# Kernel optimization log

Hardware: AMD Instinct MI355X
Metric: run time of the kernel (lower is better)

Reference implementation:

```python
import jax, jax.numpy as jnp
import numpy as np

H = 1024      # hidden_size
NH = 16       # num_heads
DK = H // NH  # head dim


def setup_inputs() -> dict:
    key = jax.random.key(0)
    ks = jax.random.split(key, 5)
    s = 0.02
    return {
        "x": jax.random.normal(ks[0], (4, 2048, H), dtype=jnp.float32),
        "W_attn": jax.random.normal(ks[1], (H, 3 * H), dtype=jnp.float32) * s,
        "b_attn": jnp.zeros((3 * H,), dtype=jnp.float32),
        "W_proj": jax.random.normal(ks[2], (H, H), dtype=jnp.float32) * s,
        "b_proj": jnp.zeros((H,), dtype=jnp.float32),
    }


def reference(x, W_attn, b_attn, W_proj, b_proj):
    B, S, _ = x.shape
    qkv = x @ W_attn + b_attn                      # [B,S,3H]
    q, k, v = jnp.split(qkv, 3, axis=-1)
    # split heads -> [B,NH,S,DK]
    def heads(t):
        return t.reshape(B, S, NH, DK).transpose(0, 2, 1, 3)
    q, k, v = heads(q), heads(k), heads(v)
    scores = jnp.einsum("bhqd,bhkd->bhqk", q, k) / jnp.sqrt(jnp.float32(DK))
    causal = jnp.triu(jnp.full((S, S), -jnp.inf, dtype=scores.dtype), k=1)
    scores = scores + causal                        # additive causal mask
    attn = jax.nn.softmax(scores, axis=-1)
    out = jnp.einsum("bhqk,bhkd->bhqd", attn, v)   # [B,NH,S,DK]
    out = out.transpose(0, 2, 1, 3).reshape(B, S, H)
    return out @ W_proj + b_proj
```

## Files before the change

kernel.cpp:

```cpp
#include <hip/hip_runtime.h>
#include <hip/hip_bf16.h>


typedef __attribute__((ext_vector_type(8))) short bhalf8;
typedef __attribute__((ext_vector_type(4))) float floatx4;
typedef __attribute__((ext_vector_type(16))) float floatx16;

#define SB 2048
#define HB 1024
#define H3 3072

#if __has_builtin(__builtin_amdgcn_exp2f)
#define EXP2(x) __builtin_amdgcn_exp2f(x)
#else
#define EXP2(x) exp2f(x)
#endif

__device__ __forceinline__ float bf2f(unsigned short u) {
  union { unsigned int i; float f; } c; c.i = ((unsigned int)u) << 16; return c.f;
}
__device__ __forceinline__ unsigned short f2bf(float f) {
  union { float f; unsigned int i; } c; c.f = f;
  unsigned int r = c.i + 0x7fffu + ((c.i >> 16) & 1u);
  return (unsigned short)(r >> 16);
}
__device__ __forceinline__ int pkbf(float lo, float hi_) {
  union { __hip_bfloat162 h; int i; } u;
  u.h = __float22bfloat162_rn(make_float2(lo, hi_));
  return u.i;
}

__device__ __forceinline__ void gl_lds16(const unsigned short* g, unsigned short* l) {
  __builtin_amdgcn_global_load_lds(
      (const __attribute__((address_space(1))) unsigned int*)g,
      (__attribute__((address_space(3))) unsigned int*)l, 16, 0, 0);
}

#define REP16(OP) OP(0) OP(1) OP(2) OP(3) OP(4) OP(5) OP(6) OP(7) \
                  OP(8) OP(9) OP(10) OP(11) OP(12) OP(13) OP(14) OP(15)

__global__ void cvt_f32_bf16(const float* __restrict__ in, unsigned short* __restrict__ out, int n) {
  int i = (blockIdx.x * blockDim.x + threadIdx.x) * 4;
  if (i >= n) return;
  float4 v = *(const float4*)(in + i);
  ushort4 o;
  o.x = f2bf(v.x); o.y = f2bf(v.y); o.z = f2bf(v.z); o.w = f2bf(v.w);
  *(ushort4*)(out + i) = o;
}

__global__ void transpose_cvt(const float* __restrict__ in, unsigned short* __restrict__ out,
                              int K, int N) {
  __shared__ float tile[32][33];
  int n0 = blockIdx.x * 32, k0 = blockIdx.y * 32;
  for (int i = threadIdx.y; i < 32; i += 8)
    tile[i][threadIdx.x] = in[(size_t)(k0 + i) * N + n0 + threadIdx.x];
  __syncthreads();
  for (int i = threadIdx.y; i < 32; i += 8)
    out[(size_t)(n0 + i) * K + k0 + threadIdx.x] = f2bf(tile[threadIdx.x][i]);
}

__global__ void transpose_v(const unsigned short* __restrict__ qkv,
                            unsigned short* __restrict__ Vt) {
  __shared__ unsigned short tile[32][33];
  const int bh = blockIdx.z;
  const int b = bh >> 4, h = bh & 15;
  const int s0 = blockIdx.x * 32;
  const int d0 = blockIdx.y * 32;
  const int tx = threadIdx.x;
  const unsigned short* src = qkv + (size_t)(b * SB + s0) * H3 + 2 * HB + h * 64 + d0;
  for (int i = threadIdx.y; i < 32; i += 8)
    tile[i][tx] = src[(size_t)i * H3 + tx];
  __syncthreads();
  unsigned short* dst = Vt + ((size_t)bh * 64 + d0) * SB + s0;
  for (int i = threadIdx.y; i < 32; i += 8)
    dst[(size_t)i * SB + tx] = tile[tx][i];
}

template <bool FUSEV>
__global__ __launch_bounds__(512, 2) void gemm_v9(
    const unsigned short* __restrict__ A,
    const unsigned short* __restrict__ Bt,
    const float* __restrict__ bias,
    unsigned short* __restrict__ C,
    unsigned short* __restrict__ Vt,
    int M, int N, int K) {
  __shared__ __align__(16) unsigned short Sm[3 * 20480];
  const int tid = threadIdx.x;
  const int lane = tid & 63;
  const int w = tid >> 6;
  const int l15 = lane & 15, l4 = lane >> 4;
  const int wm = w >> 2, wn = w & 3;

  const int gx = gridDim.x;
  int lin = blockIdx.y * gx + blockIdx.x;
  const int cpx = (gx * gridDim.y) >> 3;
  lin = (lin & 7) * cpx + (lin >> 3);
  const int m0 = (lin / gx) * 256;
  const int n0 = (lin % gx) * 384;

  const int rb0 = tid >> 2;
  const int co = (((tid & 3) ^ ((tid >> 3) & 3)) * 8);
  const unsigned short* pA0 = A + (size_t)(m0 + rb0) * K + co;
  const unsigned short* pA1 = pA0 + (size_t)128 * K;
  const unsigned short* pB0 = Bt + (size_t)(n0 + rb0) * K + co;
  const unsigned short* pB1 = pB0 + (size_t)128 * K;
  const unsigned short* pB2 = pB0 + (size_t)256 * K;

  const int ra0 = wm * 128 + l15;
  const int ab0 = ra0 * 64 + ((l4 ^ ((ra0 >> 1) & 3)) << 4);
  const int rbq = wn * 96 + l15;
  const int bb0 = 16384 + rbq * 64 + ((l4 ^ ((rbq >> 1) & 3)) << 4);

  const floatx4 zero = {0.f, 0.f, 0.f, 0.f};
  floatx4 acc[8][6];
#pragma unroll
  for (int i = 0; i < 8; ++i)
#pragma unroll
    for (int j = 0; j < 6; ++j) acc[i][j] = zero;

#define STAGE_A(k0, ss)                                                 \
  { gl_lds16(pA0 + (k0), Sm + (ss) + tid * 8);                          \
    gl_lds16(pA1 + (k0), Sm + (ss) + (tid + 512) * 8); }
#define STAGE_B(k0, ss)                                                 \
  { gl_lds16(pB0 + (k0), Sm + (ss) + 8192 + tid * 8);                   \
    gl_lds16(pB1 + (k0), Sm + (ss) + 8192 + (tid + 512) * 8);           \
    gl_lds16(pB2 + (k0), Sm + (ss) + 8192 + (tid + 1024) * 8); }

  const int NT = K >> 5;
  STAGE_A(0, 0)      STAGE_B(0, 0)
  STAGE_A(32, 20480) STAGE_B(32, 20480)
  int sb = 0;
  int ss = 40960;

  for (int t = 0; t < NT; ++t) {
    if (t < NT - 1) asm volatile("s_waitcnt vmcnt(5)" ::: "memory");
    else            asm volatile("s_waitcnt vmcnt(0)" ::: "memory");
    __builtin_amdgcn_s_barrier();

    const char* LB = (const char*)(Sm + sb);
    const int k2 = (t + 2) * 32;
    const bool st = (t + 2 < NT);

    bhalf8 a0 = *(const bhalf8*)(LB + ab0);
    bhalf8 a1 = *(const bhalf8*)(LB + ab0 + 1024);
    bhalf8 a2 = *(const bhalf8*)(LB + ab0 + 2048);
    bhalf8 a3 = *(const bhalf8*)(LB + ab0 + 3072);
    bhalf8 b0 = *(const bhalf8*)(LB + bb0);
    bhalf8 b1 = *(const bhalf8*)(LB + bb0 + 1024);
    bhalf8 b2 = *(const bhalf8*)(LB + bb0 + 2048);
    bhalf8 b3 = *(const bhalf8*)(LB + bb0 + 3072);
    bhalf8 b4 = *(const bhalf8*)(LB + bb0 + 4096);
    bhalf8 b5 = *(const bhalf8*)(LB + bb0 + 5120);
    if (st) STAGE_A(k2, ss)
    __builtin_amdgcn_s_setprio(1);
#define MROW(i, av)                                                              \
    acc[i][0] = __builtin_amdgcn_mfma_f32_16x16x32_bf16(av, b0, acc[i][0], 0, 0, 0); \
    acc[i][1] = __builtin_amdgcn_mfma_f32_16x16x32_bf16(av, b1, acc[i][1], 0, 0, 0); \
    acc[i][2] = __builtin_amdgcn_mfma_f32_16x16x32_bf16(av, b2, acc[i][2], 0, 0, 0); \
    acc[i][3] = __builtin_amdgcn_mfma_f32_16x16x32_bf16(av, b3, acc[i][3], 0, 0, 0); \
    acc[i][4] = __builtin_amdgcn_mfma_f32_16x16x32_bf16(av, b4, acc[i][4], 0, 0, 0); \
    acc[i][5] = __builtin_amdgcn_mfma_f32_16x16x32_bf16(av, b5, acc[i][5], 0, 0, 0);
    MROW(0, a0) MROW(1, a1) MROW(2, a2) MROW(3, a3)
    __builtin_amdgcn_s_setprio(0);
    __builtin_amdgcn_s_barrier();

    bhalf8 a4 = *(const bhalf8*)(LB + ab0 + 4096);
    bhalf8 a5 = *(const bhalf8*)(LB + ab0 + 5120);
    bhalf8 a6 = *(const bhalf8*)(LB + ab0 + 6144);
    bhalf8 a7 = *(const bhalf8*)(LB + ab0 + 7168);
    if (st) STAGE_B(k2, ss)
    __builtin_amdgcn_s_setprio(1);
    MROW(4, a4) MROW(5, a5) MROW(6, a6) MROW(7, a7)
#undef MROW
    __builtin_amdgcn_s_setprio(0);

    sb = (sb == 40960) ? 0 : sb + 20480;
    ss = (ss == 40960) ? 0 : ss + 20480;
  }
#undef STAGE_A
#undef STAGE_B

#pragma unroll
  for (int i = 0; i < 8; ++i) {
    int row = m0 + wm * 128 + i * 16 + (l4 << 2);
#pragma unroll
    for (int j = 0; j < 6; ++j) {
      int col = n0 + wn * 96 + j * 16 + l15;
      float bb = bias[col];
      if (!FUSEV || col < 2048) {
#pragma unroll
        for (int r = 0; r < 4; ++r)
          C[(size_t)(row + r) * N + col] = f2bf(acc[i][j][r] + bb);
      } else {
        int vc = col - 2048;
        int h = vc >> 6, dk = vc & 63;
        int b = row >> 11, s = row & 2047;
        ushort4 pv;
        pv.x = f2bf(acc[i][j][0] + bb);
        pv.y = f2bf(acc[i][j][1] + bb);
        pv.z = f2bf(acc[i][j][2] + bb);
        pv.w = f2bf(acc[i][j][3] + bb);
        *(ushort4*)(Vt + ((size_t)((b * 16 + h) * 64 + dk)) * SB + s) = pv;
      }
    }
  }
}

template <bool F32OUT>
__global__ __launch_bounds__(512, 4) void gemm_v6(
    const unsigned short* __restrict__ A,
    const unsigned short* __restrict__ Bt,
    const float* __restrict__ bias,
    void* __restrict__ Cv,
    int M, int N, int K) {
  __shared__ __align__(16) unsigned short Sm[3 * 12288];
  const int tid = threadIdx.x;
  const int lane = tid & 63;
  const int w = tid >> 6;
  const int l15 = lane & 15, l4 = lane >> 4;
  const int wr = (w >> 1) * 64;
  const int wc = (w & 1) * 64;

  const int gx = gridDim.x;
  int lin = blockIdx.y * gx + blockIdx.x;
  const int cpx = (gx * gridDim.y) >> 3;
  lin = (lin & 7) * cpx + (lin >> 3);
  const int m0 = (lin / gx) * 256;
  const int n0 = (lin % gx) * 128;

  const int idx0 = tid, idx1 = tid + 512;
  const unsigned short* pA0 = A + (size_t)(m0 + (idx0 >> 2)) * K + (((idx0 & 3) ^ ((idx0 >> 3) & 3)) * 8);
  const unsigned short* pA1 = A + (size_t)(m0 + (idx1 >> 2)) * K + (((idx1 & 3) ^ ((idx1 >> 3) & 3)) * 8);
  const unsigned short* pB  = Bt + (size_t)(n0 + (tid >> 2)) * K + (((tid & 3) ^ ((tid >> 3) & 3)) * 8);

  int abyte[4], bbyte[4];
#pragma unroll
  for (int i = 0; i < 4; ++i) {
    int ra = wr + i * 16 + l15;
    abyte[i] = ra * 64 + ((l4 ^ ((ra >> 1) & 3)) << 4);
    int rb = wc + i * 16 + l15;
    bbyte[i] = 16384 + rb * 64 + ((l4 ^ ((rb >> 1) & 3)) << 4);
  }

  const floatx4 zero = {0.f, 0.f, 0.f, 0.f};
  floatx4 acc[4][4];
#pragma unroll
  for (int i = 0; i < 4; ++i)
#pragma unroll
    for (int j = 0; j < 4; ++j) acc[i][j] = zero;

#define STAGE_A6(k0, sbase)                                             \
  { gl_lds16(pA0 + (k0), Sm + (sbase) + idx0 * 8);                      \
    gl_lds16(pA1 + (k0), Sm + (sbase) + idx1 * 8); }
#define STAGE_B6(k0, sbase)                                             \
  { gl_lds16(pB + (k0), Sm + (sbase) + 8192 + tid * 8); }

  const int NT = K >> 5;
  STAGE_A6(0, 0)  STAGE_B6(0, 0)
  STAGE_A6(32, 12288) STAGE_B6(32, 12288)
  int sb = 0;
  int ss = 24576;

  for (int t = 0; t < NT; ++t) {
    if (t < NT - 1) asm volatile("s_waitcnt vmcnt(3)" ::: "memory");
    else            asm volatile("s_waitcnt vmcnt(0)" ::: "memory");
    __builtin_amdgcn_s_barrier();

    const char* LB = (const char*)(Sm + sb);
    const int k2 = (t + 2) * 32;
    const bool st = (t + 2 < NT);

    bhalf8 a0 = *(const bhalf8*)(LB + abyte[0]);
    bhalf8 a1 = *(const bhalf8*)(LB + abyte[1]);
    bhalf8 b0 = *(const bhalf8*)(LB + bbyte[0]);
    bhalf8 b1 = *(const bhalf8*)(LB + bbyte[1]);
    bhalf8 b2 = *(const bhalf8*)(LB + bbyte[2]);
    bhalf8 b3 = *(const bhalf8*)(LB + bbyte[3]);
    if (st) STAGE_A6(k2, ss)
    __builtin_amdgcn_s_setprio(1);
    acc[0][0] = __builtin_amdgcn_mfma_f32_16x16x32_bf16(a0, b0, acc[0][0], 0, 0, 0);
    acc[0][1] = __builtin_amdgcn_mfma_f32_16x16x32_bf16(a0, b1, acc[0][1], 0, 0, 0);
    acc[0][2] = __builtin_amdgcn_mfma_f32_16x16x32_bf16(a0, b2, acc[0][2], 0, 0, 0);
    acc[0][3] = __builtin_amdgcn_mfma_f32_16x16x32_bf16(a0, b3, acc[0][3], 0, 0, 0);
    acc[1][0] = __builtin_amdgcn_mfma_f32_16x16x32_bf16(a1, b0, acc[1][0], 0, 0, 0);
    acc[1][1] = __builtin_amdgcn_mfma_f32_16x16x32_bf16(a1, b1, acc[1][1], 0, 0, 0);
    acc[1][2] = __builtin_amdgcn_mfma_f32_16x16x32_bf16(a1, b2, acc[1][2], 0, 0, 0);
    acc[1][3] = __builtin_amdgcn_mfma_f32_16x16x32_bf16(a1, b3, acc[1][3], 0, 0, 0);
    __builtin_amdgcn_s_setprio(0);
    __builtin_amdgcn_s_barrier();

    bhalf8 a2 = *(const bhalf8*)(LB + abyte[2]);
    bhalf8 a3 = *(const bhalf8*)(LB + abyte[3]);
    if (st) STAGE_B6(k2, ss)
    __builtin_amdgcn_s_setprio(1);
    acc[2][0] = __builtin_amdgcn_mfma_f32_16x16x32_bf16(a2, b0, acc[2][0], 0, 0, 0);
    acc[2][1] = __builtin_amdgcn_mfma_f32_16x16x32_bf16(a2, b1, acc[2][1], 0, 0, 0);
    acc[2][2] = __builtin_amdgcn_mfma_f32_16x16x32_bf16(a2, b2, acc[2][2], 0, 0, 0);
    acc[2][3] = __builtin_amdgcn_mfma_f32_16x16x32_bf16(a2, b3, acc[2][3], 0, 0, 0);
    acc[3][0] = __builtin_amdgcn_mfma_f32_16x16x32_bf16(a3, b0, acc[3][0], 0, 0, 0);
    acc[3][1] = __builtin_amdgcn_mfma_f32_16x16x32_bf16(a3, b1, acc[3][1], 0, 0, 0);
    acc[3][2] = __builtin_amdgcn_mfma_f32_16x16x32_bf16(a3, b2, acc[3][2], 0, 0, 0);
    acc[3][3] = __builtin_amdgcn_mfma_f32_16x16x32_bf16(a3, b3, acc[3][3], 0, 0, 0);
    __builtin_amdgcn_s_setprio(0);

    sb = (sb == 24576) ? 0 : sb + 12288;
    ss = (ss == 24576) ? 0 : ss + 12288;
  }
#undef STAGE_A6
#undef STAGE_B6

  float* Cf = (float*)Cv;
  unsigned short* Cb = (unsigned short*)Cv;
#pragma unroll
  for (int i = 0; i < 4; ++i) {
    int row = m0 + wr + i * 16 + (l4 << 2);
#pragma unroll
    for (int j = 0; j < 4; ++j) {
      int col = n0 + wc + j * 16 + l15;
      float bb = bias[col];
#pragma unroll
      for (int r = 0; r < 4; ++r) {
        float v = acc[i][j][r] + bb;
        size_t idx = (size_t)(row + r) * N + col;
        if constexpr (F32OUT) Cf[idx] = v;
        else Cb[idx] = f2bf(v);
      }
    }
  }
}

__global__ __launch_bounds__(256, 4) void flash_attn4(
    const unsigned short* __restrict__ qkv,
    const unsigned short* __restrict__ Vt,
    unsigned short* __restrict__ outp) {
  __shared__ __align__(16) unsigned short Sm[4 * 4096];

  const int tid = threadIdx.x;
  const int lane = tid & 63;
  const int w = tid >> 6;
  const int hi = lane >> 5;
  const int qc = lane & 31;
  const int bh = blockIdx.x;
  const int b = bh >> 4, h = bh & 15;
  const int qt = 15 - (int)blockIdx.y;
  const int wq0 = qt * 128 + w * 32;
  const size_t rowbase = (size_t)b * SB;
  const int qg = wq0 + qc;
  const int nt = 2 * qt + 2;

  bhalf8 qf[4];
  {
    const unsigned short* qp = qkv + (rowbase + qg) * H3 + h * 64 + hi * 8;
#pragma unroll
    for (int kk = 0; kk < 4; ++kk) {
      bhalf8 v = *(const bhalf8*)(qp + kk * 16);
      bhalf8 o;
#pragma unroll
      for (int j = 0; j < 8; ++j)
        o[j] = (short)f2bf(bf2f((unsigned short)v[j]) * 0.18033688f);
      qf[kk] = o;
    }
  }

  const floatx16 Z16 = {0,0,0,0,0,0,0,0,0,0,0,0,0,0,0,0};
  floatx16 acc0 = Z16, acc1 = Z16;
  float l_half = 0.f;

  const char* LB = (const char*)Sm;
  int koff[8];
#pragma unroll
  for (int kk = 0; kk < 4; ++kk) {
    int xo = (((2 * kk + hi) ^ (qc & 7)) << 4);
    koff[2 * kk]     = qc * 128 + xo;
    koff[2 * kk + 1] = (32 + qc) * 128 + xo;
  }

  const int srow = tid >> 3, schk = tid & 7;
  const int sxe = (schk ^ (srow & 7)) * 8;
  const unsigned short* kp = qkv + (rowbase + srow) * H3 + HB + h * 64 + sxe;
  const unsigned short* vp = Vt + ((size_t)bh * 64 + srow) * SB + sxe;

  {
    unsigned short* kb = Sm + tid * 8;
    gl_lds16(kp, kb);
    gl_lds16(kp + 32 * H3, kb + 2048);
    gl_lds16(vp, kb + 8192);
    gl_lds16(vp + 32 * SB, kb + 8192 + 2048);
  }

#define QKK(BUFB, kk)                                                              \
      { bhalf8 ka = *(const bhalf8*)(LB + (BUFB) + koff[2*(kk)]);                  \
        s0 = __builtin_amdgcn_mfma_f32_32x32x16_bf16(ka, qf[kk], s0, 0, 0, 0);     \
        bhalf8 kb2 = *(const bhalf8*)(LB + (BUFB) + koff[2*(kk)+1]);               \
        s1 = __builtin_amdgcn_mfma_f32_32x32x16_bf16(kb2, qf[kk], s1, 0, 0, 0); }
#define PVC(BUFB, c, pfv)                                                          \
      { bhalf8 va = *(const bhalf8*)(LB + 16384 + (BUFB) + koff[2*(c)]);           \
        acc0 = __builtin_amdgcn_mfma_f32_32x32x16_bf16(va, pfv, acc0, 0, 0, 0);    \
        bhalf8 vb2 = *(const bhalf8*)(LB + 16384 + (BUFB) + koff[2*(c)+1]);        \
        acc1 = __builtin_amdgcn_mfma_f32_32x32x16_bf16(vb2, pfv, acc1, 0, 0, 0); }
#define MSK0(r) { if (k0 + (((r)&3) + 8*((r)>>2)) + 4*hi > qg)      s0[r] = -3.0e38f; }
#define MSK1(r) { if (k0 + 32 + (((r)&3) + 8*((r)>>2)) + 4*hi > qg) s1[r] = -3.0e38f; }
#define PEXP(r) { s0[r] = EXP2(s0[r]); s1[r] = EXP2(s1[r]); rsx[(r)&3] += s0[r] + s1[r]; }
  union PW { int i[4]; bhalf8 v; };
#define PACK2(dst, sv, rb)                                               \
      { int A0 = pkbf(sv[rb + 0], sv[rb + 1]);                           \
        int A1 = pkbf(sv[rb + 2], sv[rb + 3]);                           \
        int B0 = pkbf(sv[rb + 4], sv[rb + 5]);                           \
        int B1 = pkbf(sv[rb + 6], sv[rb + 7]);                           \
        auto r0 = __builtin_amdgcn_permlane32_swap(A0, B0, false, false);\
        auto r1 = __builtin_amdgcn_permlane32_swap(A1, B1, false, false);\
        PW u;                                                            \
        u.i[0] = r0[0]; u.i[1] = r1[0];                                  \
        u.i[2] = r0[1]; u.i[3] = r1[1];                                  \
        dst = u.v; }

#define FLASH_COMPUTE(BUFB)                                                        \
    { floatx16 s0 = Z16, s1 = Z16;                                                 \
      __builtin_amdgcn_s_setprio(1);                                               \
      QKK(BUFB, 0) QKK(BUFB, 1) QKK(BUFB, 2) QKK(BUFB, 3)                          \
      __builtin_amdgcn_s_setprio(0);                                               \
      if (k0 + 63 > wq0) { REP16(MSK0) REP16(MSK1) }                               \
      float rsx[4] = {0.f, 0.f, 0.f, 0.f};                                         \
      REP16(PEXP)                                                                  \
      l_half += (rsx[0] + rsx[1]) + (rsx[2] + rsx[3]);                             \
      bhalf8 pf0, pf1, pf2, pf3;                                                   \
      PACK2(pf0, s0, 0) PACK2(pf1, s0, 8) PACK2(pf2, s1, 0) PACK2(pf3, s1, 8)      \
      __builtin_amdgcn_s_setprio(1);                                               \
      PVC(BUFB, 0, pf0) PVC(BUFB, 1, pf1) PVC(BUFB, 2, pf2) PVC(BUFB, 3, pf3)      \
      __builtin_amdgcn_s_setprio(0); }

#define DO_STEP(T, BUF)                                                            \
  { __syncthreads();                                                               \
    if ((T) + 1 < nt) {                                                            \
      kp += 64 * H3; vp += 64;                                                     \
      unsigned short* kb = Sm + (1 - (BUF)) * 4096 + tid * 8;                      \
      gl_lds16(kp, kb); gl_lds16(kp + 32 * H3, kb + 2048);                         \
      gl_lds16(vp, kb + 8192); gl_lds16(vp + 32 * SB, kb + 8192 + 2048);           \
    }                                                                              \
    const int k0 = (T) * 64;                                                       \
    if (k0 <= wq0 + 31) FLASH_COMPUTE((BUF) * 8192)                                \
  }

  for (int t = 0; t < nt; t += 2) {
    DO_STEP(t, 0)
    DO_STEP(t + 1, 1)
  }

  const float l_full = l_half + __shfl_xor(l_half, 32);
  const float inv_l = 1.f / l_full;
  unsigned short* op = outp + (rowbase + qg) * HB + h * 64;
#pragma unroll
  for (int tq = 0; tq < 4; ++tq) {
    ushort4 st;
    st.x = f2bf(acc0[4 * tq + 0] * inv_l);
    st.y = f2bf(acc0[4 * tq + 1] * inv_l);
    st.z = f2bf(acc0[4 * tq + 2] * inv_l);
    st.w = f2bf(acc0[4 * tq + 3] * inv_l);
    *(ushort4*)(op + 8 * tq + 4 * hi) = st;
    ushort4 su;
    su.x = f2bf(acc1[4 * tq + 0] * inv_l);
    su.y = f2bf(acc1[4 * tq + 1] * inv_l);
    su.z = f2bf(acc1[4 * tq + 2] * inv_l);
    su.w = f2bf(acc1[4 * tq + 3] * inv_l);
    *(ushort4*)(op + 32 + 8 * tq + 4 * hi) = su;
  }
}

extern "C" void kernel_launch(void* const* d_in, const int* in_sizes, int n_in,
                              void* d_out, int out_size, void* d_ws, size_t ws_size,
                              hipStream_t stream) {
  const float* x      = (const float*)d_in[0];
  const float* W_attn = (const float*)d_in[1];
  const float* b_attn = (const float*)d_in[2];
  const float* W_proj = (const float*)d_in[3];
  const float* b_proj = (const float*)d_in[4];
  float* out = (float*)d_out;

  char* ws = (char*)d_ws;
  unsigned short* x_bf    = (unsigned short*)(ws);
  unsigned short* Wt_attn = (unsigned short*)(ws + 16777216);
  unsigned short* Wt_proj = (unsigned short*)(ws + 23068672);
  unsigned short* qkv     = (unsigned short*)(ws + 25165824);
  unsigned short* attn    = (unsigned short*)(ws + 75497472);
  const bool fuse = ws_size >= (size_t)92274688 + 16777216;
  unsigned short* VtF = (unsigned short*)(ws + 92274688);
  unsigned short* Vt  = fuse ? VtF : x_bf;

  cvt_f32_bf16<<<8192, 256, 0, stream>>>(x, x_bf, 8192 * 1024);
  transpose_cvt<<<dim3(96, 32), dim3(32, 8), 0, stream>>>(W_attn, Wt_attn, 1024, 3072);
  transpose_cvt<<<dim3(32, 32), dim3(32, 8), 0, stream>>>(W_proj, Wt_proj, 1024, 1024);

  if (fuse) {
    gemm_v9<true><<<dim3(8, 32), 512, 0, stream>>>(x_bf, Wt_attn, b_attn, qkv, VtF,
                                                   8192, 3072, 1024);
  } else {
    gemm_v9<false><<<dim3(8, 32), 512, 0, stream>>>(x_bf, Wt_attn, b_attn, qkv, nullptr,
                                                    8192, 3072, 1024);
    transpose_v<<<dim3(64, 2, 64), dim3(32, 8), 0, stream>>>(qkv, Vt);
  }
  flash_attn4<<<dim3(64, 16), 256, 0, stream>>>(qkv, Vt, attn);
  gemm_v6<true><<<dim3(8, 32), 512, 0, stream>>>(attn, Wt_proj, b_proj, out,
                                                 8192, 1024, 1024);
}
```

Measured before the change: 145.9 us.

## Triple-buffer K/V tiles in flash attention with explicit vmcnt waits

Replaces the double-buffered K/V LDS staging in the attention kernel with a three-stage ring. Loads run two tiles ahead, and partial s_waitcnt vmcnt waits replace the full __syncthreads drain. The goal is to hide global-to-LDS load latency behind the MFMA compute. In exchange it uses 48KB of LDS per block and lowers the launch-bound occupancy hint from 4 to 3 blocks.

```diff
diff --git a/kernel.cpp b/kernel.cpp
--- a/kernel.cpp
+++ b/kernel.cpp
@@ -193,14 +193,14 @@
           C[(size_t)(row + r) * N + col] = f2bf(acc[i][j][r] + bb);
       } else {
         int vc = col - 2048;
-        int h = vc >> 6, dk = vc & 63;
-        int b = row >> 11, s = row & 2047;
+        int h2 = vc >> 6, dk = vc & 63;
+        int b2 = row >> 11, s = row & 2047;
         ushort4 pv;
         pv.x = f2bf(acc[i][j][0] + bb);
         pv.y = f2bf(acc[i][j][1] + bb);
         pv.z = f2bf(acc[i][j][2] + bb);
         pv.w = f2bf(acc[i][j][3] + bb);
-        *(ushort4*)(Vt + ((size_t)((b * 16 + h) * 64 + dk)) * SB + s) = pv;
+        *(ushort4*)(Vt + ((size_t)((b2 * 16 + h2) * 64 + dk)) * SB + s) = pv;
       }
     }
   }
@@ -329,11 +329,11 @@
   }
 }
 
-__global__ __launch_bounds__(256, 4) void flash_attn4(
+__global__ __launch_bounds__(256, 3) void flash_attn5(
     const unsigned short* __restrict__ qkv,
     const unsigned short* __restrict__ Vt,
     unsigned short* __restrict__ outp) {
-  __shared__ __align__(16) unsigned short Sm[4 * 4096];
+  __shared__ __align__(16) unsigned short Sm[3 * 8192];
 
   const int tid = threadIdx.x;
   const int lane = tid & 63;
@@ -366,7 +366,6 @@
   floatx16 acc0 = Z16, acc1 = Z16;
   float l_half = 0.f;
 
-  const char* LB = (const char*)Sm;
   int koff[8];
 #pragma unroll
   for (int kk = 0; kk < 4; ++kk) {
@@ -380,28 +379,53 @@
   const unsigned short* kp = qkv + (rowbase + srow) * H3 + HB + h * 64 + sxe;
   const unsigned short* vp = Vt + ((size_t)bh * 64 + srow) * SB + sxe;
 
-  {
-    unsigned short* kb = Sm + tid * 8;
-    gl_lds16(kp, kb);
-    gl_lds16(kp + 32 * H3, kb + 2048);
-    gl_lds16(vp, kb + 8192);
-    gl_lds16(vp + 32 * SB, kb + 8192 + 2048);
-  }
-
-#define QKK(BUFB, kk)                                                              \
-      { bhalf8 ka = *(const bhalf8*)(LB + (BUFB) + koff[2*(kk)]);                  \
-        s0 = __builtin_amdgcn_mfma_f32_32x32x16_bf16(ka, qf[kk], s0, 0, 0, 0);     \
-        bhalf8 kb2 = *(const bhalf8*)(LB + (BUFB) + koff[2*(kk)+1]);               \
-        s1 = __builtin_amdgcn_mfma_f32_32x32x16_bf16(kb2, qf[kk], s1, 0, 0, 0); }
-#define PVC(BUFB, c, pfv)                                                          \
-      { bhalf8 va = *(const bhalf8*)(LB + 16384 + (BUFB) + koff[2*(c)]);           \
-        acc0 = __builtin_amdgcn_mfma_f32_32x32x16_bf16(va, pfv, acc0, 0, 0, 0);    \
-        bhalf8 vb2 = *(const bhalf8*)(LB + 16384 + (BUFB) + koff[2*(c)+1]);        \
-        acc1 = __builtin_amdgcn_mfma_f32_32x32x16_bf16(vb2, pfv, acc1, 0, 0, 0); }
+#define STG(CS, KO)                                                              \
+  { unsigned short* kb = Sm + (CS) + tid * 8;                                    \
+    gl_lds16(kp + (size_t)(KO) * H3,        kb);                                 \
+    gl_lds16(kp + (size_t)((KO) + 32) * H3, kb + 2048);                          \
+    gl_lds16(vp + (KO),            kb + 4096);                                   \
+    gl_lds16(vp + (KO) + 32 * SB,  kb + 6144); }
+
+  STG(0, 0)
+  STG(8192, 64)
+  int cmp = 0;
+  int stg = 16384;
+
+  for (int t = 0; t < nt; ++t) {
+    if (t < nt - 1) asm volatile("s_waitcnt vmcnt(4)" ::: "memory");
+    else            asm volatile("s_waitcnt vmcnt(0)" ::: "memory");
+    __builtin_amdgcn_s_barrier();
+
+    if (t + 2 < nt) STG(stg, (t + 2) * 64)
+
+    const int k0 = t * 64;
+    if (k0 <= wq0 + 31) {
+      const char* Lc = (const char*)Sm + cmp * 2;
+
+      floatx16 s0 = Z16, s1 = Z16;
+      __builtin_amdgcn_s_setprio(1);
+#pragma unroll
+      for (int kk = 0; kk < 4; ++kk) {
+        bhalf8 ka  = *(const bhalf8*)(Lc + koff[2 * kk]);
+        s0 = __builtin_amdgcn_mfma_f32_32x32x16_bf16(ka, qf[kk], s0, 0, 0, 0);
+        bhalf8 kb2 = *(const bhalf8*)(Lc + koff[2 * kk + 1]);
+        s1 = __builtin_amdgcn_mfma_f32_32x32x16_bf16(kb2, qf[kk], s1, 0, 0, 0);
+      }
+      __builtin_amdgcn_s_setprio(0);
+
+      if (k0 + 63 > wq0) {
 #define MSK0(r) { if (k0 + (((r)&3) + 8*((r)>>2)) + 4*hi > qg)      s0[r] = -3.0e38f; }
 #define MSK1(r) { if (k0 + 32 + (((r)&3) + 8*((r)>>2)) + 4*hi > qg) s1[r] = -3.0e38f; }
+        REP16(MSK0)
+        REP16(MSK1)
+      }
+
+      float rsx[4] = {0.f, 0.f, 0.f, 0.f};
 #define PEXP(r) { s0[r] = EXP2(s0[r]); s1[r] = EXP2(s1[r]); rsx[(r)&3] += s0[r] + s1[r]; }
-  union PW { int i[4]; bhalf8 v; };
+      REP16(PEXP)
+      l_half += (rsx[0] + rsx[1]) + (rsx[2] + rsx[3]);
+
+      union PW { int i[4]; bhalf8 v; };
 #define PACK2(dst, sv, rb)                                               \
       { int A0 = pkbf(sv[rb + 0], sv[rb + 1]);                           \
         int A1 = pkbf(sv[rb + 2], sv[rb + 3]);                           \
@@ -413,38 +437,30 @@
         u.i[0] = r0[0]; u.i[1] = r1[0];                                  \
         u.i[2] = r0[1]; u.i[3] = r1[1];                                  \
         dst = u.v; }
-
-#define FLASH_COMPUTE(BUFB)                                                        \
-    { floatx16 s0 = Z16, s1 = Z16;                                                 \
-      __builtin_amdgcn_s_setprio(1);                                               \
-      QKK(BUFB, 0) QKK(BUFB, 1) QKK(BUFB, 2) QKK(BUFB, 3)                          \
-      __builtin_amdgcn_s_setprio(0);                                               \
-      if (k0 + 63 > wq0) { REP16(MSK0) REP16(MSK1) }                               \
-      float rsx[4] = {0.f, 0.f, 0.f, 0.f};                                         \
-      REP16(PEXP)                                                                  \
-      l_half += (rsx[0] + rsx[1]) + (rsx[2] + rsx[3]);                             \
-      bhalf8 pf0, pf1, pf2, pf3;                                                   \
-      PACK2(pf0, s0, 0) PACK2(pf1, s0, 8) PACK2(pf2, s1, 0) PACK2(pf3, s1, 8)      \
-      __builtin_amdgcn_s_setprio(1);                                               \
-      PVC(BUFB, 0, pf0) PVC(BUFB, 1, pf1) PVC(BUFB, 2, pf2) PVC(BUFB, 3, pf3)      \
-      __builtin_amdgcn_s_setprio(0); }
-
-#define DO_STEP(T, BUF)                                                            \
-  { __syncthreads();                                                               \
-    if ((T) + 1 < nt) {                                                            \
-      kp += 64 * H3; vp += 64;                                                     \
-      unsigned short* kb = Sm + (1 - (BUF)) * 4096 + tid * 8;                      \
-      gl_lds16(kp, kb); gl_lds16(kp + 32 * H3, kb + 2048);                         \
-      gl_lds16(vp, kb + 8192); gl_lds16(vp + 32 * SB, kb + 8192 + 2048);           \
-    }                                                                              \
-    const int k0 = (T) * 64;                                                       \
-    if (k0 <= wq0 + 31) FLASH_COMPUTE((BUF) * 8192)                                \
-  }
-
-  for (int t = 0; t < nt; t += 2) {
-    DO_STEP(t, 0)
-    DO_STEP(t + 1, 1)
-  }
+      bhalf8 pf0, pf1, pf2, pf3;
+      PACK2(pf0, s0, 0)
+      PACK2(pf1, s0, 8)
+      PACK2(pf2, s1, 0)
+      PACK2(pf3, s1, 8)
+
+      __builtin_amdgcn_s_setprio(1);
+#define PVC(c, pfv)                                                                  \
+      { bhalf8 va  = *(const bhalf8*)(Lc + 8192 + koff[2 * (c)]);                    \
+        acc0 = __builtin_amdgcn_mfma_f32_32x32x16_bf16(va, pfv, acc0, 0, 0, 0);      \
+        bhalf8 vb2 = *(const bhalf8*)(Lc + 8192 + koff[2 * (c) + 1]);                \
+        acc1 = __builtin_amdgcn_mfma_f32_32x32x16_bf16(vb2, pfv, acc1, 0, 0, 0); }
+      PVC(0, pf0)
+      PVC(1, pf1)
+      PVC(2, pf2)
+      PVC(3, pf3)
+      __builtin_amdgcn_s_setprio(0);
+#undef PVC
+    }
+
+    cmp = (cmp == 16384) ? 0 : cmp + 8192;
+    stg = (stg == 16384) ? 0 : stg + 8192;
+  }
+#undef STG
 
   const float l_full = l_half + __shfl_xor(l_half, 32);
   const float inv_l = 1.f / l_full;
@@ -498,7 +514,7 @@
                                                     8192, 3072, 1024);
     transpose_v<<<dim3(64, 2, 64), dim3(32, 8), 0, stream>>>(qkv, Vt);
   }
-  flash_attn4<<<dim3(64, 16), 256, 0, stream>>>(qkv, Vt, attn);
+  flash_attn5<<<dim3(64, 16), 256, 0, stream>>>(qkv, Vt, attn);
   gemm_v6<true><<<dim3(8, 32), 512, 0, stream>>>(attn, Wt_proj, b_proj, out,
                                                  8192, 1024, 1024);
 }
```

After: 148.8 us. About the same (+2.0%).
